# Performance work log

Measured on AMD Instinct MI355X. Metric: run time of the kernel, lower is better.

## Reference

```python
import jax, jax.numpy as jnp
import numpy as np

B, S, HID = 2, 2048, 1024
H, D = 16, 64
NUM_BUCKETS, MAX_DIST = 32, 128
NEG_INF = -1e9


def _rel_buckets(rel_pos, num_buckets, max_distance):
    # decoder (unidirectional): only non-positive relative positions valid
    rp = -jnp.minimum(rel_pos, 0)  # [q,k] >= 0
    max_exact = num_buckets // 2
    is_small = rp < max_exact
    safe = jnp.maximum(rp, 1).astype(jnp.float32)
    large = max_exact + (
        jnp.log(safe / max_exact) / np.log(max_distance / max_exact) * (num_buckets - max_exact)
    ).astype(jnp.int32)
    large = jnp.minimum(large, num_buckets - 1)
    return jnp.where(is_small, rp, large)


def _rotate_half(t):
    t1, t2 = jnp.split(t, 2, axis=-1)
    return jnp.concatenate([-t2, t1], axis=-1)


def setup_inputs() -> dict:
    key = jax.random.key(0)
    ks = jax.random.split(key, 6)
    sc = 0.02
    x = jax.random.normal(ks[0], (B, S, HID), jnp.float32)
    Wq = jax.random.normal(ks[1], (HID, H * D), jnp.float32) * sc
    Wk = jax.random.normal(ks[2], (HID, H * D), jnp.float32) * sc
    Wv = jax.random.normal(ks[3], (HID, H * D), jnp.float32) * sc
    Wo = jax.random.normal(ks[4], (H * D, HID), jnp.float32) * sc
    rel_bias = jax.random.normal(ks[5], (NUM_BUCKETS, H), jnp.float32) * sc
    # rotary tables: emb = cat(freqs, freqs), non-interleave layout
    inv_freq = 1.0 / (10000.0 ** (np.arange(0, D, 2, dtype=np.float32) / D))
    freqs = np.arange(S, dtype=np.float32)[:, None] * inv_freq[None, :]  # [S, D/2]
    emb = np.concatenate([freqs, freqs], axis=-1)  # [S, D]
    cos = jnp.asarray(np.cos(emb), jnp.float32)
    sin = jnp.asarray(np.sin(emb), jnp.float32)
    return {"x": x, "Wq": Wq, "Wk": Wk, "Wv": Wv, "Wo": Wo,
            "rel_bias": rel_bias, "cos": cos, "sin": sin}


def reference(x, Wq, Wk, Wv, Wo, rel_bias, cos, sin):
    # QKV projections (weights stored [in, out])
    q = (x @ Wq).reshape(B, S, H, D)
    k = (x @ Wk).reshape(B, S, H, D)
    v = (x @ Wv).reshape(B, S, H, D)
    # RoPE (non-interleave): q*cos + rotate_half(q)*sin, cos/sin broadcast over B,H
    c = cos[None, :, None, :]
    s = sin[None, :, None, :]
    q = q * c + _rotate_half(q) * s
    k = k * c + _rotate_half(k) * s
    # scores [B,H,S,S]
    scores = jnp.einsum("bqhd,bkhd->bhqk", q, k) / np.sqrt(D).astype(np.float32)
    # learned relative-position bucket bias (T5-style, decoder/unidirectional)
    ctx_pos = jnp.arange(S)[:, None]
    mem_pos = jnp.arange(S)[None, :]
    buckets = _rel_buckets(mem_pos - ctx_pos, NUM_BUCKETS, MAX_DIST)  # [S,S]
    bias = rel_bias[buckets]  # [S,S,H]
    scores = scores + jnp.transpose(bias, (2, 0, 1))[None]
    # causal mask (decoder self-attention)
    causal = mem_pos <= ctx_pos  # [S,S]
    scores = jnp.where(causal[None, None], scores, NEG_INF)
    attn = jax.nn.softmax(scores, axis=-1)
    ctx = jnp.einsum("bhqk,bkhd->bqhd", attn, v).reshape(B, S, H * D)
    return ctx @ Wo
```

## Files before the change

kernel.cpp:

```cpp
#include <hip/hip_runtime.h>
#include <hip/hip_bf16.h>
#include <math.h>

#define B_   2
#define S_   2048
#define HID_ 1024
#define H_   16
#define D_   64

typedef __attribute__((ext_vector_type(8))) short bf16x8;
typedef __attribute__((ext_vector_type(4))) short bf16x4;
typedef __attribute__((ext_vector_type(4))) float f32x4;
typedef __attribute__((ext_vector_type(4))) unsigned uint4v;
typedef unsigned short u16;

#define LOG2E 1.44269504088896f

static __device__ __forceinline__ u16 f2bf(float f) {
    unsigned u = __builtin_bit_cast(unsigned, f);
    u += 0x7fffu + ((u >> 16) & 1u);
    return (u16)(u >> 16);
}
static __device__ __forceinline__ unsigned cvtpk(float lo, float hi) {
    unsigned r;
    asm("v_cvt_pk_bf16_f32 %0, %1, %2" : "=v"(r) : "v"(lo), "v"(hi));
    return r;
}
static __device__ __forceinline__ int swzK(int row, int colbytes) {
    return row * 128 + (colbytes ^ ((row & 7) << 4));
}
static __device__ __forceinline__ int swzV(int row, int colbytes) {
    return row * 128 + (colbytes ^ ((row & 7) << 4) ^ (((row >> 3) & 1) << 3));
}
static __device__ __forceinline__ void gll16(const void* g, void* l) {
    __builtin_amdgcn_global_load_lds(
        (const __attribute__((address_space(1))) unsigned int*)g,
        (__attribute__((address_space(3))) unsigned int*)l, 16, 0, 0);
}

__global__ __launch_bounds__(256) void convert_x(const float* __restrict__ in,
                                                 u16* __restrict__ out) {
    int i = blockIdx.x * 256 + threadIdx.x;
    float4 f = ((const float4*)in)[i];
    ushort4 u;
    u.x = f2bf(f.x); u.y = f2bf(f.y); u.z = f2bf(f.z); u.w = f2bf(f.w);
    ((ushort4*)out)[i] = u;
}

__global__ __launch_bounds__(256) void transpose_w4(const float* __restrict__ W0,
                                                    const float* __restrict__ W1,
                                                    const float* __restrict__ W2,
                                                    const float* __restrict__ W3,
                                                    u16* __restrict__ o0,
                                                    u16* __restrict__ o1,
                                                    u16* __restrict__ o2,
                                                    u16* __restrict__ o3) {
    __shared__ float tS[32][33];
    const int z = blockIdx.z;
    const float* in = z == 0 ? W0 : z == 1 ? W1 : z == 2 ? W2 : W3;
    u16* out       = z == 0 ? o0 : z == 1 ? o1 : z == 2 ? o2 : o3;
    const int x = threadIdx.x, y = threadIdx.y;
    const int bx = blockIdx.x * 32, by = blockIdx.y * 32;
    #pragma unroll
    for (int j = 0; j < 4; j++)
        tS[y + j * 8][x] = in[(long)(by + y + j * 8) * HID_ + bx + x];
    __syncthreads();
    #pragma unroll
    for (int j = 0; j < 4; j++)
        out[(long)(bx + y + j * 8) * HID_ + by + x] = f2bf(tS[x][y + j * 8]);
}

__global__ __launch_bounds__(256, 3) void gemm_qkv(const u16* __restrict__ A,
                                                   const u16* __restrict__ Bt,
                                                   u16* __restrict__ outb,
                                                   const float* __restrict__ cosb,
                                                   const float* __restrict__ sinb,
                                                   int K) {
    __shared__ u16 As[128 * 32];
    __shared__ u16 Bs[128 * 32];
    const int t = threadIdx.x;
    const int lane = t & 63;
    const int w = t >> 6;
    const int qlane = lane & 15, grp = lane >> 4;
    const int m0 = blockIdx.y * 128, n0 = blockIdx.x * 128;
    const int wr = w >> 1, wc = w & 1;

    f32x4 acc[4][4];
    #pragma unroll
    for (int i = 0; i < 4; i++)
        #pragma unroll
        for (int j = 0; j < 4; j++) acc[i][j] = (f32x4){0.f, 0.f, 0.f, 0.f};

    const int srow = (lane >> 2);
    const int scol = (lane & 3) * 8;
    const int nkt = K >> 5;
    for (int kt = 0; kt < nkt; kt++) {
        const int k0 = kt << 5;
        #pragma unroll
        for (int c = 0; c < 2; c++) {
            const int chunk = w * 2 + c;
            const int row = chunk * 16 + srow;
            gll16(A  + (long)(m0 + row) * K + k0 + scol, As + chunk * 512);
            gll16(Bt + (long)(n0 + row) * K + k0 + scol, Bs + chunk * 512);
        }
        __syncthreads();
        bf16x8 af[4], bfr[4];
        #pragma unroll
        for (int i = 0; i < 4; i++) {
            af[i]  = *(const bf16x8*)(As + (wr * 64 + i * 16 + qlane) * 32 + grp * 8);
            bfr[i] = *(const bf16x8*)(Bs + (wc * 64 + i * 16 + qlane) * 32 + grp * 8);
        }
        #pragma unroll
        for (int mf = 0; mf < 4; mf++)
            #pragma unroll
            for (int nf = 0; nf < 4; nf++)
                acc[mf][nf] = __builtin_amdgcn_mfma_f32_16x16x32_bf16(bfr[nf], af[mf], acc[mf][nf], 0, 0, 0);
        __syncthreads();
    }

    const int gnb = n0 + wc * 64;
    const bool isqk = gnb < 2048;
    const bool isq  = gnb < 1024;
    const float QS = 0.125f * LOG2E;
    #pragma unroll
    for (int mf = 0; mf < 4; mf++) {
        const int m = m0 + wr * 64 + mf * 16 + qlane;
        if (isqk) {
            const int s = m & (S_ - 1);
            const float* cr = cosb + s * 64;
            const float* sr = sinb + s * 64;
            #pragma unroll
            for (int nf2 = 0; nf2 < 2; nf2++) {
                #pragma unroll
                for (int r = 0; r < 4; r++) {
                    const int d = nf2 * 16 + grp * 4 + r;
                    float lo = acc[mf][nf2][r], hi = acc[mf][nf2 + 2][r];
                    float nlo = lo * cr[d]      - hi * sr[d];
                    float nhi = hi * cr[d + 32] + lo * sr[d + 32];
                    if (isq) { nlo *= QS; nhi *= QS; }
                    acc[mf][nf2][r]     = nlo;
                    acc[mf][nf2 + 2][r] = nhi;
                }
            }
        }
        #pragma unroll
        for (int nf = 0; nf < 4; nf++) {
            const int gn = gnb + nf * 16 + grp * 4;
            ushort4 o4;
            o4.x = f2bf(acc[mf][nf][0]); o4.y = f2bf(acc[mf][nf][1]);
            o4.z = f2bf(acc[mf][nf][2]); o4.w = f2bf(acc[mf][nf][3]);
            *(ushort4*)&outb[((long)(gn >> 10)) * ((long)4096 * 1024) + (long)m * 1024 + (gn & 1023)] = o4;
        }
    }
}

__global__ __launch_bounds__(256, 3) void gemm_n64(const u16* __restrict__ A,
                                                   const u16* __restrict__ Bt,
                                                   float* __restrict__ outf,
                                                   int K) {
    __shared__ u16 As[128 * 32];
    __shared__ u16 Bs[64 * 32];
    const int t = threadIdx.x;
    const int lane = t & 63;
    const int w = t >> 6;
    const int qlane = lane & 15, grp = lane >> 4;
    const int m0 = blockIdx.y * 128, n0 = blockIdx.x * 64;

    f32x4 acc[2][4];
    #pragma unroll
    for (int i = 0; i < 2; i++)
        #pragma unroll
        for (int j = 0; j < 4; j++) acc[i][j] = (f32x4){0.f, 0.f, 0.f, 0.f};

    const int srow = (lane >> 2);
    const int scol = (lane & 3) * 8;
    const int nkt = K >> 5;
    for (int kt = 0; kt < nkt; kt++) {
        const int k0 = kt << 5;
        #pragma unroll
        for (int c = 0; c < 2; c++) {
            const int chunk = w * 2 + c;
            const int row = chunk * 16 + srow;
            gll16(A + (long)(m0 + row) * K + k0 + scol, As + chunk * 512);
        }
        gll16(Bt + (long)(n0 + w * 16 + srow) * K + k0 + scol, Bs + w * 512);
        __syncthreads();
        bf16x8 af[2], bfr[4];
        #pragma unroll
        for (int i = 0; i < 2; i++)
            af[i] = *(const bf16x8*)(As + (w * 32 + i * 16 + qlane) * 32 + grp * 8);
        #pragma unroll
        for (int i = 0; i < 4; i++)
            bfr[i] = *(const bf16x8*)(Bs + (i * 16 + qlane) * 32 + grp * 8);
        #pragma unroll
        for (int mf = 0; mf < 2; mf++)
            #pragma unroll
            for (int nf = 0; nf < 4; nf++)
                acc[mf][nf] = __builtin_amdgcn_mfma_f32_16x16x32_bf16(bfr[nf], af[mf], acc[mf][nf], 0, 0, 0);
        __syncthreads();
    }

    #pragma unroll
    for (int mf = 0; mf < 2; mf++) {
        const int m = m0 + w * 32 + mf * 16 + qlane;
        #pragma unroll
        for (int nf = 0; nf < 4; nf++) {
            float4 o4;
            o4.x = acc[mf][nf][0]; o4.y = acc[mf][nf][1];
            o4.z = acc[mf][nf][2]; o4.w = acc[mf][nf][3];
            *(float4*)&outf[(long)m * 1024 + n0 + nf * 16 + grp * 4] = o4;
        }
    }
}

__global__ __launch_bounds__(512, 4) void attn_mfma(const u16* __restrict__ q,
                                                    const u16* __restrict__ k,
                                                    const u16* __restrict__ v,
                                                    const float* __restrict__ rel_bias,
                                                    u16* __restrict__ ctx) {
    __shared__ __align__(16) unsigned char kS[2][8192];
    __shared__ __align__(16) unsigned char vS[2][8192];
    __shared__ float bb[2][192];

    const int t    = threadIdx.x;
    const int lane = t & 63;
    const int w    = t >> 6;
    const int n    = blockIdx.x;
    const int xcd  = n & 7;
    const int hbhi = (n >> 7) & 3;
    int qtb        = (n >> 3) & 15;
    if (hbhi & 2) qtb = 15 - qtb;
    const int hb   = xcd + (hbhi << 3);
    const int h    = hb & 15, b = hb >> 4;
    const int q0   = qtb * 128;
    const int wq   = w * 16;
    const int qwq  = q0 + wq;
    const int qlane = lane & 15;
    const int grp   = lane >> 4;

    const long bhbase = ((long)b * S_ * H_ + h) * D_;
    const float bfar  = rel_bias[31 * H_ + h] * LOG2E;

    const int kr  = t >> 3,        kc  = (t & 7) * 8;
    const int vrb = (t >> 5) * 4,  vcp = (t & 31) * 2;

    bf16x8 qf0, qf1;
    {
        const u16* qrow = q + bhbase + (long)(qwq + qlane) * (H_ * D_);
        qf0 = *(const bf16x8*)(qrow + grp * 8);
        qf1 = *(const bf16x8*)(qrow + 32 + grp * 8);
    }

    f32x4 oacc[4];
    #pragma unroll
    for (int db = 0; db < 4; db++) oacc[db] = (f32x4){0.f, 0.f, 0.f, 0.f};
    float m_run = -1.0e30f, l_run = 0.f;

    bf16x8 kreg;
    unsigned vreg[4];
    float breg = 0.f;

    auto prefetch = [&](int k0, bool needb) {
        kreg = *(const bf16x8*)(k + bhbase + (long)(k0 + kr) * (H_ * D_) + kc);
        const u16* vp = v + bhbase + (long)(k0 + vrb) * (H_ * D_) + vcp;
        #pragma unroll
        for (int i = 0; i < 4; i++)
            vreg[i] = *(const unsigned*)(vp + (long)i * (H_ * D_));
        if (needb && t < 192) {
            int rp = (q0 - 63) + t - k0;
            float bv = 0.f;
            if (rp >= 0) {
                int bucket;
                if (rp < 16) bucket = rp;
                else {
                    int lg = (int)(logf((float)rp * 0.0625f) * 7.69437361f);
                    bucket = 16 + lg;
                    if (bucket > 31) bucket = 31;
                }
                bv = rel_bias[bucket * H_ + h] * LOG2E;
            }
            breg = bv;
        }
    };
    auto writetile = [&](int buf, bool needb) {
        *(bf16x8*)(kS[buf] + swzK(kr, kc * 2)) = kreg;
        ushort2 a0 = __builtin_bit_cast(ushort2, vreg[0]);
        ushort2 a1 = __builtin_bit_cast(ushort2, vreg[1]);
        ushort2 a2 = __builtin_bit_cast(ushort2, vreg[2]);
        ushort2 a3 = __builtin_bit_cast(ushort2, vreg[3]);
        ushort4 d0; d0.x = a0.x; d0.y = a1.x; d0.z = a2.x; d0.w = a3.x;
        ushort4 d1; d1.x = a0.y; d1.y = a1.y; d1.z = a2.y; d1.w = a3.y;
        *(ushort4*)(vS[buf] + swzV(vcp,     vrb * 2)) = d0;
        *(ushort4*)(vS[buf] + swzV(vcp + 1, vrb * 2)) = d1;
        if (needb && t < 192) bb[buf][t] = breg;
    };

    const int NT = 2 * qtb + 2;
    const bool needb0 = (q0 < 176);
    prefetch(0, needb0);
    writetile(0, needb0);
    __syncthreads();

    int cur = 0;
    for (int kt = 0; kt < NT; kt++) {
        const int k0 = kt * 64;
        const bool has_next = (kt + 1) < NT;
        const bool needb_n  = (q0 - (k0 + 64)) < 176;
        if (has_next) prefetch(k0 + 64, needb_n);

        const bool skip = k0 > qwq + 15;
        if (!skip) {
            const bool use_bias = (qwq - k0) < 176;
            const bool is_diag  = (k0 + 63) > qwq;

            __builtin_amdgcn_s_setprio(1);
            f32x4 sacc[4];
            #pragma unroll
            for (int kb = 0; kb < 4; kb++) {
                sacc[kb] = (f32x4){0.f, 0.f, 0.f, 0.f};
                bf16x8 kf0 = *(const bf16x8*)(kS[cur] + swzK(kb * 16 + qlane, grp * 16));
                bf16x8 kf1 = *(const bf16x8*)(kS[cur] + swzK(kb * 16 + qlane, 64 + grp * 16));
                sacc[kb] = __builtin_amdgcn_mfma_f32_16x16x32_bf16(kf0, qf0, sacc[kb], 0, 0, 0);
                sacc[kb] = __builtin_amdgcn_mfma_f32_16x16x32_bf16(kf1, qf1, sacc[kb], 0, 0, 0);
            }
            __builtin_amdgcn_s_setprio(0);

            float pv_[4][4];
            float tmax = -1.0e30f;
            #pragma unroll
            for (int kb = 0; kb < 4; kb++) {
                #pragma unroll
                for (int r = 0; r < 4; r++) {
                    float s = sacc[kb][r];
                    if (use_bias) {
                        const int k_l = kb * 16 + grp * 4 + r;
                        s += bb[cur][wq + qlane - k_l + 63];
                        if (is_diag)
                            s = ((k0 + k_l) <= (qwq + qlane)) ? s : -1.0e9f;
                    }
                    pv_[kb][r] = s;
                }
                tmax = fmaxf(tmax,
                       fmaxf(fmaxf(pv_[kb][0], pv_[kb][1]), fmaxf(pv_[kb][2], pv_[kb][3])));
            }
            tmax = fmaxf(tmax, __shfl_xor(tmax, 16));
            tmax = fmaxf(tmax, __shfl_xor(tmax, 32));

            const float bofs = use_bias ? 0.f : bfar;
            const float teff = tmax + bofs;
            float msub;
            if (__all(teff <= m_run + 11.5f)) {
                msub = m_run - bofs;
            } else {
                float mnew  = fmaxf(m_run, teff);
                float scale = __builtin_amdgcn_exp2f(m_run - mnew);
                l_run *= scale;
                #pragma unroll
                for (int db = 0; db < 4; db++)
                    #pragma unroll
                    for (int r = 0; r < 4; r++) oacc[db][r] *= scale;
                m_run = mnew;
                msub = mnew - bofs;
            }

            float tsum = 0.f;
            #pragma unroll
            for (int kb = 0; kb < 4; kb++)
                #pragma unroll
                for (int r = 0; r < 4; r++) {
                    float p = __builtin_amdgcn_exp2f(pv_[kb][r] - msub);
                    pv_[kb][r] = p;
                    tsum += p;
                }
            tsum += __shfl_xor(tsum, 16);
            tsum += __shfl_xor(tsum, 32);
            l_run += tsum;

            bf16x8 pf[2];
            #pragma unroll
            for (int ks = 0; ks < 2; ks++) {
                unsigned u0 = cvtpk(pv_[2 * ks][0], pv_[2 * ks][1]);
                unsigned u1 = cvtpk(pv_[2 * ks][2], pv_[2 * ks][3]);
                unsigned u2 = cvtpk(pv_[2 * ks + 1][0], pv_[2 * ks + 1][1]);
                unsigned u3 = cvtpk(pv_[2 * ks + 1][2], pv_[2 * ks + 1][3]);
                pf[ks] = __builtin_bit_cast(bf16x8, (uint4v){u0, u1, u2, u3});
            }

            __builtin_amdgcn_s_setprio(1);
            #pragma unroll
            for (int db = 0; db < 4; db++) {
                #pragma unroll
                for (int ks = 0; ks < 2; ks++) {
                    bf16x4 lo = *(const bf16x4*)(vS[cur] + swzV(db * 16 + qlane, ks * 64 + grp * 8));
                    bf16x4 hi = *(const bf16x4*)(vS[cur] + swzV(db * 16 + qlane, ks * 64 + 32 + grp * 8));
                    bf16x8 vf = __builtin_shufflevector(lo, hi, 0, 1, 2, 3, 4, 5, 6, 7);
                    oacc[db] = __builtin_amdgcn_mfma_f32_16x16x32_bf16(vf, pf[ks], oacc[db], 0, 0, 0);
                }
            }
            __builtin_amdgcn_s_setprio(0);
        }

        if (has_next) writetile(cur ^ 1, needb_n);
        __syncthreads();
        cur ^= 1;
    }

    const float inv = 1.0f / l_run;
    u16* dst = ctx + (long)(b * S_ + qwq + qlane) * HID_ + h * D_;
    #pragma unroll
    for (int db = 0; db < 4; db++) {
        ushort4 o4;
        o4.x = f2bf(oacc[db][0] * inv);
        o4.y = f2bf(oacc[db][1] * inv);
        o4.z = f2bf(oacc[db][2] * inv);
        o4.w = f2bf(oacc[db][3] * inv);
        *(ushort4*)(dst + db * 16 + grp * 4) = o4;
    }
}

extern "C" void kernel_launch(void* const* d_in, const int* in_sizes, int n_in,
                              void* d_out, int out_size, void* d_ws, size_t ws_size,
                              hipStream_t stream) {
    const float* x    = (const float*)d_in[0];
    const float* Wq   = (const float*)d_in[1];
    const float* Wk   = (const float*)d_in[2];
    const float* Wv   = (const float*)d_in[3];
    const float* Wo   = (const float*)d_in[4];
    const float* rb   = (const float*)d_in[5];
    const float* cosb = (const float*)d_in[6];
    const float* sinb = (const float*)d_in[7];
    float* out = (float*)d_out;

    char* wsb = (char*)d_ws;
    u16* xb    = (u16*)(wsb);
    u16* wqkvT = (u16*)(wsb + (8L  << 20));
    u16* woT   = (u16*)(wsb + (14L << 20));
    u16* qb    = (u16*)(wsb + (16L << 20));
    u16* kb    = (u16*)(wsb + (24L << 20));
    u16* vb    = (u16*)(wsb + (32L << 20));
    u16* ctxb  = (u16*)(wsb + (40L << 20));

    hipLaunchKernelGGL(convert_x, dim3((B_ * S_ * HID_ / 4) / 256), dim3(256), 0, stream, x, xb);
    hipLaunchKernelGGL(transpose_w4, dim3(32, 32, 4), dim3(32, 8), 0, stream,
                       Wq, Wk, Wv, Wo,
                       wqkvT, wqkvT + (1L << 20), wqkvT + (2L << 20), woT);

    hipLaunchKernelGGL(gemm_qkv, dim3(24, 32), dim3(256), 0, stream,
                       xb, wqkvT, qb, cosb, sinb, HID_);
    hipLaunchKernelGGL(attn_mfma, dim3(512), dim3(512), 0, stream,
                       qb, kb, vb, rb, ctxb);
    hipLaunchKernelGGL(gemm_n64, dim3(16, 32), dim3(256), 0, stream,
                       ctxb, woT, out, HID_);
}
```

Measured before the change: 125.9 us.

## Process two 16-row query groups per wave and stage K via direct-to-LDS loads

The attention kernel moves from 8 waves each owning 16 query rows to 4 waves each owning 32 rows (two sets A and B). Each K and V fragment read from LDS now feeds two MFMAs, halving LDS traffic per unit of compute. K tiles are now staged with global_load_lds straight into LDS instead of going through registers, and V is loaded in wider ushort4 chunks and transposed. This costs more registers per wave (two accumulator sets) and halves the threads per block, which lowers latency hiding and causal-skip granularity.

Result: slower. 151.6 us (+20.5%).

```diff
diff --git a/kernel.cpp b/kernel.cpp
--- a/kernel.cpp
+++ b/kernel.cpp
@@ -7,6 +7,7 @@
 #define HID_ 1024
 #define H_   16
 #define D_   64
+#define HD_  (H_ * D_)
 
 typedef __attribute__((ext_vector_type(8))) short bf16x8;
 typedef __attribute__((ext_vector_type(4))) short bf16x4;
@@ -37,6 +38,7 @@
         (const __attribute__((address_space(1))) unsigned int*)g,
         (__attribute__((address_space(3))) unsigned int*)l, 16, 0, 0);
 }
+#define VCOMP(vv, j) ((j) == 0 ? (vv).x : (j) == 1 ? (vv).y : (j) == 2 ? (vv).z : (vv).w)
 
 __global__ __launch_bounds__(256) void convert_x(const float* __restrict__ in,
                                                  u16* __restrict__ out) {
@@ -213,7 +215,7 @@
     }
 }
 
-__global__ __launch_bounds__(512, 4) void attn_mfma(const u16* __restrict__ q,
+__global__ __launch_bounds__(256, 2) void attn_mfma(const u16* __restrict__ q,
                                                     const u16* __restrict__ k,
                                                     const u16* __restrict__ v,
                                                     const float* __restrict__ rel_bias,
@@ -233,39 +235,55 @@
     const int hb   = xcd + (hbhi << 3);
     const int h    = hb & 15, b = hb >> 4;
     const int q0   = qtb * 128;
-    const int wq   = w * 16;
-    const int qwq  = q0 + wq;
+    const int woff = w * 32;
+    const int qA   = q0 + woff;
+    const int qB   = qA + 16;
     const int qlane = lane & 15;
     const int grp   = lane >> 4;
 
     const long bhbase = ((long)b * S_ * H_ + h) * D_;
     const float bfar  = rel_bias[31 * H_ + h] * LOG2E;
 
-    const int kr  = t >> 3,        kc  = (t & 7) * 8;
-    const int vrb = (t >> 5) * 4,  vcp = (t & 31) * 2;
-
-    bf16x8 qf0, qf1;
+    const int krow8 = lane >> 3;
+    const int kc16  = (lane & 7) ^ krow8;
+    const u16* kp0 = k + bhbase + (long)(w * 16 + krow8) * HD_ + kc16 * 8;
+    const u16* kp1 = kp0 + (long)8 * HD_;
+
+    const int vrb = (t >> 4) * 4;
+    const int vcp = (t & 15) * 4;
+    const u16* vpb = v + bhbase + (long)vrb * HD_ + vcp;
+
+    bf16x8 qfA0, qfA1, qfB0, qfB1;
     {
-        const u16* qrow = q + bhbase + (long)(qwq + qlane) * (H_ * D_);
-        qf0 = *(const bf16x8*)(qrow + grp * 8);
-        qf1 = *(const bf16x8*)(qrow + 32 + grp * 8);
-    }
-
-    f32x4 oacc[4];
-    #pragma unroll
-    for (int db = 0; db < 4; db++) oacc[db] = (f32x4){0.f, 0.f, 0.f, 0.f};
-    float m_run = -1.0e30f, l_run = 0.f;
-
-    bf16x8 kreg;
-    unsigned vreg[4];
+        const u16* qr = q + bhbase + (long)(qA + qlane) * HD_;
+        qfA0 = *(const bf16x8*)(qr + grp * 8);
+        qfA1 = *(const bf16x8*)(qr + 32 + grp * 8);
+        qr += (long)16 * HD_;
+        qfB0 = *(const bf16x8*)(qr + grp * 8);
+        qfB1 = *(const bf16x8*)(qr + 32 + grp * 8);
+    }
+
+    f32x4 oA[4], oB[4];
+    #pragma unroll
+    for (int db = 0; db < 4; db++) {
+        oA[db] = (f32x4){0.f, 0.f, 0.f, 0.f};
+        oB[db] = (f32x4){0.f, 0.f, 0.f, 0.f};
+    }
+    float mA = -1.0e30f, lA = 0.f, mB = -1.0e30f, lB = 0.f;
+
+    ushort4 vreg[4];
     float breg = 0.f;
-
-    auto prefetch = [&](int k0, bool needb) {
-        kreg = *(const bf16x8*)(k + bhbase + (long)(k0 + kr) * (H_ * D_) + kc);
-        const u16* vp = v + bhbase + (long)(k0 + vrb) * (H_ * D_) + vcp;
+    int cur = 0;
+
+    auto stageK = [&](int k0, int buf) {
+        gll16(kp0 + (long)k0 * HD_, kS[buf] + (w * 2) * 1024);
+        gll16(kp1 + (long)k0 * HD_, kS[buf] + (w * 2 + 1) * 1024);
+    };
+    auto prefetchV = [&](int k0, bool needb) {
+        const u16* vp = vpb + (long)k0 * HD_;
         #pragma unroll
         for (int i = 0; i < 4; i++)
-            vreg[i] = *(const unsigned*)(vp + (long)i * (H_ * D_));
+            vreg[i] = *(const ushort4*)(vp + (long)i * HD_);
         if (needb && t < 192) {
             int rp = (q0 - 63) + t - k0;
             float bv = 0.f;
@@ -282,109 +300,122 @@
             breg = bv;
         }
     };
-    auto writetile = [&](int buf, bool needb) {
-        *(bf16x8*)(kS[buf] + swzK(kr, kc * 2)) = kreg;
-        ushort2 a0 = __builtin_bit_cast(ushort2, vreg[0]);
-        ushort2 a1 = __builtin_bit_cast(ushort2, vreg[1]);
-        ushort2 a2 = __builtin_bit_cast(ushort2, vreg[2]);
-        ushort2 a3 = __builtin_bit_cast(ushort2, vreg[3]);
-        ushort4 d0; d0.x = a0.x; d0.y = a1.x; d0.z = a2.x; d0.w = a3.x;
-        ushort4 d1; d1.x = a0.y; d1.y = a1.y; d1.z = a2.y; d1.w = a3.y;
-        *(ushort4*)(vS[buf] + swzV(vcp,     vrb * 2)) = d0;
-        *(ushort4*)(vS[buf] + swzV(vcp + 1, vrb * 2)) = d1;
+    auto writeV = [&](int buf, bool needb) {
+        #pragma unroll
+        for (int j = 0; j < 4; j++) {
+            ushort4 tc;
+            tc.x = VCOMP(vreg[0], j); tc.y = VCOMP(vreg[1], j);
+            tc.z = VCOMP(vreg[2], j); tc.w = VCOMP(vreg[3], j);
+            *(ushort4*)(vS[buf] + swzV(vcp + j, vrb * 2)) = tc;
+        }
         if (needb && t < 192) bb[buf][t] = breg;
     };
 
+    auto softmax_set = [&](f32x4* sacc, float& m_run, float& l_run, f32x4* oacc,
+                           int qoff, bool use_bias, bool is_diag, int k0,
+                           bf16x8* pf) {
+        float pv_[4][4];
+        float tmax = -1.0e30f;
+        #pragma unroll
+        for (int kb = 0; kb < 4; kb++) {
+            #pragma unroll
+            for (int r = 0; r < 4; r++) {
+                float s = sacc[kb][r];
+                if (use_bias) {
+                    const int k_l = kb * 16 + grp * 4 + r;
+                    s += bb[cur][qoff + qlane - k_l + 63];
+                    if (is_diag)
+                        s = ((k0 + k_l) <= (q0 + qoff + qlane)) ? s : -1.0e9f;
+                }
+                pv_[kb][r] = s;
+            }
+            tmax = fmaxf(tmax,
+                   fmaxf(fmaxf(pv_[kb][0], pv_[kb][1]), fmaxf(pv_[kb][2], pv_[kb][3])));
+        }
+        tmax = fmaxf(tmax, __shfl_xor(tmax, 16));
+        tmax = fmaxf(tmax, __shfl_xor(tmax, 32));
+
+        const float bofs = use_bias ? 0.f : bfar;
+        const float teff = tmax + bofs;
+        float msub;
+        if (__all(teff <= m_run + 11.5f)) {
+            msub = m_run - bofs;
+        } else {
+            float mnew  = fmaxf(m_run, teff);
+            float scale = __builtin_amdgcn_exp2f(m_run - mnew);
+            l_run *= scale;
+            #pragma unroll
+            for (int db = 0; db < 4; db++)
+                #pragma unroll
+                for (int r = 0; r < 4; r++) oacc[db][r] *= scale;
+            m_run = mnew;
+            msub = mnew - bofs;
+        }
+
+        float tsum = 0.f;
+        #pragma unroll
+        for (int kb = 0; kb < 4; kb++)
+            #pragma unroll
+            for (int r = 0; r < 4; r++) {
+                float p = __builtin_amdgcn_exp2f(pv_[kb][r] - msub);
+                pv_[kb][r] = p;
+                tsum += p;
+            }
+        tsum += __shfl_xor(tsum, 16);
+        tsum += __shfl_xor(tsum, 32);
+        l_run += tsum;
+
+        #pragma unroll
+        for (int ks = 0; ks < 2; ks++) {
+            unsigned u0 = cvtpk(pv_[2 * ks][0], pv_[2 * ks][1]);
+            unsigned u1 = cvtpk(pv_[2 * ks][2], pv_[2 * ks][3]);
+            unsigned u2 = cvtpk(pv_[2 * ks + 1][0], pv_[2 * ks + 1][1]);
+            unsigned u3 = cvtpk(pv_[2 * ks + 1][2], pv_[2 * ks + 1][3]);
+            pf[ks] = __builtin_bit_cast(bf16x8, (uint4v){u0, u1, u2, u3});
+        }
+    };
+
     const int NT = 2 * qtb + 2;
     const bool needb0 = (q0 < 176);
-    prefetch(0, needb0);
-    writetile(0, needb0);
+    stageK(0, 0);
+    prefetchV(0, needb0);
+    writeV(0, needb0);
     __syncthreads();
 
-    int cur = 0;
     for (int kt = 0; kt < NT; kt++) {
         const int k0 = kt * 64;
         const bool has_next = (kt + 1) < NT;
         const bool needb_n  = (q0 - (k0 + 64)) < 176;
-        if (has_next) prefetch(k0 + 64, needb_n);
-
-        const bool skip = k0 > qwq + 15;
+        if (has_next) {
+            stageK(k0 + 64, cur ^ 1);
+            prefetchV(k0 + 64, needb_n);
+        }
+
+        const bool skip = k0 > qB + 15;
         if (!skip) {
-            const bool use_bias = (qwq - k0) < 176;
-            const bool is_diag  = (k0 + 63) > qwq;
+            const bool biasA = (qA - k0) < 176;
+            const bool biasB = (qB - k0) < 176;
+            const bool diagA = (k0 + 63) > qA;
+            const bool diagB = (k0 + 63) > qB;
 
             __builtin_amdgcn_s_setprio(1);
-            f32x4 sacc[4];
+            f32x4 sA[4], sB[4];
             #pragma unroll
             for (int kb = 0; kb < 4; kb++) {
-                sacc[kb] = (f32x4){0.f, 0.f, 0.f, 0.f};
+                sA[kb] = (f32x4){0.f, 0.f, 0.f, 0.f};
+                sB[kb] = (f32x4){0.f, 0.f, 0.f, 0.f};
                 bf16x8 kf0 = *(const bf16x8*)(kS[cur] + swzK(kb * 16 + qlane, grp * 16));
                 bf16x8 kf1 = *(const bf16x8*)(kS[cur] + swzK(kb * 16 + qlane, 64 + grp * 16));
-                sacc[kb] = __builtin_amdgcn_mfma_f32_16x16x32_bf16(kf0, qf0, sacc[kb], 0, 0, 0);
-                sacc[kb] = __builtin_amdgcn_mfma_f32_16x16x32_bf16(kf1, qf1, sacc[kb], 0, 0, 0);
+                sA[kb] = __builtin_amdgcn_mfma_f32_16x16x32_bf16(kf0, qfA0, sA[kb], 0, 0, 0);
+                sA[kb] = __builtin_amdgcn_mfma_f32_16x16x32_bf16(kf1, qfA1, sA[kb], 0, 0, 0);
+                sB[kb] = __builtin_amdgcn_mfma_f32_16x16x32_bf16(kf0, qfB0, sB[kb], 0, 0, 0);
+                sB[kb] = __builtin_amdgcn_mfma_f32_16x16x32_bf16(kf1, qfB1, sB[kb], 0, 0, 0);
             }
             __builtin_amdgcn_s_setprio(0);
 
-            float pv_[4][4];
-            float tmax = -1.0e30f;
-            #pragma unroll
-            for (int kb = 0; kb < 4; kb++) {
-                #pragma unroll
-                for (int r = 0; r < 4; r++) {
-                    float s = sacc[kb][r];
-                    if (use_bias) {
-                        const int k_l = kb * 16 + grp * 4 + r;
-                        s += bb[cur][wq + qlane - k_l + 63];
-                        if (is_diag)
-                            s = ((k0 + k_l) <= (qwq + qlane)) ? s : -1.0e9f;
-                    }
-                    pv_[kb][r] = s;
-                }
-                tmax = fmaxf(tmax,
-                       fmaxf(fmaxf(pv_[kb][0], pv_[kb][1]), fmaxf(pv_[kb][2], pv_[kb][3])));
-            }
-            tmax = fmaxf(tmax, __shfl_xor(tmax, 16));
-            tmax = fmaxf(tmax, __shfl_xor(tmax, 32));
-
-            const float bofs = use_bias ? 0.f : bfar;
-            const float teff = tmax + bofs;
-            float msub;
-            if (__all(teff <= m_run + 11.5f)) {
-                msub = m_run - bofs;
-            } else {
-                float mnew  = fmaxf(m_run, teff);
-                float scale = __builtin_amdgcn_exp2f(m_run - mnew);
-                l_run *= scale;
-                #pragma unroll
-                for (int db = 0; db < 4; db++)
-                    #pragma unroll
-                    for (int r = 0; r < 4; r++) oacc[db][r] *= scale;
-                m_run = mnew;
-                msub = mnew - bofs;
-            }
-
-            float tsum = 0.f;
-            #pragma unroll
-            for (int kb = 0; kb < 4; kb++)
-                #pragma unroll
-                for (int r = 0; r < 4; r++) {
-                    float p = __builtin_amdgcn_exp2f(pv_[kb][r] - msub);
-                    pv_[kb][r] = p;
-                    tsum += p;
-                }
-            tsum += __shfl_xor(tsum, 16);
-            tsum += __shfl_xor(tsum, 32);
-            l_run += tsum;
-
-            bf16x8 pf[2];
-            #pragma unroll
-            for (int ks = 0; ks < 2; ks++) {
-                unsigned u0 = cvtpk(pv_[2 * ks][0], pv_[2 * ks][1]);
-                unsigned u1 = cvtpk(pv_[2 * ks][2], pv_[2 * ks][3]);
-                unsigned u2 = cvtpk(pv_[2 * ks + 1][0], pv_[2 * ks + 1][1]);
-                unsigned u3 = cvtpk(pv_[2 * ks + 1][2], pv_[2 * ks + 1][3]);
-                pf[ks] = __builtin_bit_cast(bf16x8, (uint4v){u0, u1, u2, u3});
-            }
+            bf16x8 pfA[2], pfB[2];
+            softmax_set(sA, mA, lA, oA, woff,      biasA, diagA, k0, pfA);
+            softmax_set(sB, mB, lB, oB, woff + 16, biasB, diagB, k0, pfB);
 
             __builtin_amdgcn_s_setprio(1);
             #pragma unroll
@@ -394,27 +425,31 @@
                     bf16x4 lo = *(const bf16x4*)(vS[cur] + swzV(db * 16 + qlane, ks * 64 + grp * 8));
                     bf16x4 hi = *(const bf16x4*)(vS[cur] + swzV(db * 16 + qlane, ks * 64 + 32 + grp * 8));
                     bf16x8 vf = __builtin_shufflevector(lo, hi, 0, 1, 2, 3, 4, 5, 6, 7);
-                    oacc[db] = __builtin_amdgcn_mfma_f32_16x16x32_bf16(vf, pf[ks], oacc[db], 0, 0, 0);
+                    oA[db] = __builtin_amdgcn_mfma_f32_16x16x32_bf16(vf, pfA[ks], oA[db], 0, 0, 0);
+                    oB[db] = __builtin_amdgcn_mfma_f32_16x16x32_bf16(vf, pfB[ks], oB[db], 0, 0, 0);
                 }
             }
             __builtin_amdgcn_s_setprio(0);
         }
 
-        if (has_next) writetile(cur ^ 1, needb_n);
+        if (has_next) writeV(cur ^ 1, needb_n);
         __syncthreads();
         cur ^= 1;
     }
 
-    const float inv = 1.0f / l_run;
-    u16* dst = ctx + (long)(b * S_ + qwq + qlane) * HID_ + h * D_;
+    const float invA = 1.0f / lA;
+    const float invB = 1.0f / lB;
+    u16* dA = ctx + (long)(b * S_ + qA + qlane) * HID_ + h * D_;
+    u16* dB = ctx + (long)(b * S_ + qB + qlane) * HID_ + h * D_;
     #pragma unroll
     for (int db = 0; db < 4; db++) {
-        ushort4 o4;
-        o4.x = f2bf(oacc[db][0] * inv);
-        o4.y = f2bf(oacc[db][1] * inv);
-        o4.z = f2bf(oacc[db][2] * inv);
-        o4.w = f2bf(oacc[db][3] * inv);
-        *(ushort4*)(dst + db * 16 + grp * 4) = o4;
+        ushort4 a4, b4;
+        a4.x = f2bf(oA[db][0] * invA); a4.y = f2bf(oA[db][1] * invA);
+        a4.z = f2bf(oA[db][2] * invA); a4.w = f2bf(oA[db][3] * invA);
+        b4.x = f2bf(oB[db][0] * invB); b4.y = f2bf(oB[db][1] * invB);
+        b4.z = f2bf(oB[db][2] * invB); b4.w = f2bf(oB[db][3] * invB);
+        *(ushort4*)(dA + db * 16 + grp * 4) = a4;
+        *(ushort4*)(dB + db * 16 + grp * 4) = b4;
     }
 }
 
@@ -447,7 +482,7 @@
 
     hipLaunchKernelGGL(gemm_qkv, dim3(24, 32), dim3(256), 0, stream,
                        xb, wqkvT, qb, cosb, sinb, HID_);
-    hipLaunchKernelGGL(attn_mfma, dim3(512), dim3(512), 0, stream,
+    hipLaunchKernelGGL(attn_mfma, dim3(512), dim3(256), 0, stream,
                        qb, kb, vb, rb, ctxb);
     hipLaunchKernelGGL(gemm_n64, dim3(16, 32), dim3(256), 0, stream,
                        ctxb, woT, out, HID_);
```
